# Kernel optimization log

Measured on AMD Instinct MI355X. Metric: run time of the kernel, lower is better.

## Reference

```python
import jax, jax.numpy as jnp
import numpy as np

jax.config.update("jax_enable_x64", True)

N_SPINS = 32
BATCH = 64
CPLX = jnp.complex128


def gen_v_from_zz_px(zz, PX=1):
    # zz: (n,) real +/-1 values -> isometry v: (2n, n) complex
    n = zz.shape[-1]
    N = 2 * n
    sgn = jnp.sign(zz)
    sgn = sgn.at[-1].set(-PX * sgn[-1])
    norm = 1.0 / jnp.sqrt(2.0)
    top = -1j * sgn * norm
    bot = (1.0 + 0j) * norm
    a_idx = 2 * jnp.arange(n) + 1
    b_idx = (2 * jnp.arange(n) + 2) % N
    col = jnp.arange(n)
    v = jnp.zeros((N, n), dtype=CPLX)
    v = v.at[a_idx, col].set(top)
    v = v.at[b_idx, col].set(bot)
    return v


def green_function_from_two(L, R):
    Lh = jnp.swapaxes(L.conj(), -1, -2)
    M = Lh @ R
    X = jnp.linalg.solve(M, Lh)
    gbar = R @ X
    N = gbar.shape[-1]
    I = jnp.eye(N, dtype=gbar.dtype)
    return I - 2 * gbar


def gen_green_init_s_proj(s, PX=1):
    zz_val = s * jnp.roll(s, -1, axis=-1)
    v = gen_v_from_zz_px(zz_val, PX)
    return v, green_function_from_two(v, v)


def green_function_from_s_state(s, state, PX=1):
    zz_val = s * jnp.roll(s, -1, axis=-1)
    v = gen_v_from_zz_px(zz_val, PX)
    return green_function_from_two(v, state)


def _householder_n(x, n):
    # x: (N,) complex column; n traced index. Returns reflector v, tau, alpha.
    arange = jnp.arange(x.size)
    xn = x[n]
    x = jnp.where(arange <= n, jnp.zeros_like(x), x)
    sigma = jnp.vdot(x, x)
    norm_x = jnp.sqrt(xn.conj() * xn + sigma)
    phase = jnp.where(xn == 0.0, 1.0, xn / jnp.abs(xn))
    vn = xn + phase * norm_x
    alpha = -phase * norm_x
    v = jnp.where(arange == n, vn, x)
    v = v / jnp.linalg.norm(v)
    cond = sigma == 0.0
    v = jnp.where(cond, jnp.zeros_like(x), v)
    tau = jnp.where(cond, 0, 2)
    alpha = jnp.where(cond, xn, alpha)
    return v, tau, alpha


def slog_pfaffian(A):
    # Sequential Householder tridiagonalization with running sign/log tracking.
    N = A.shape[0]

    def body(carry, i):
        A, sign_val, logpf = carry
        v, tau, alpha = _householder_n(A[:, i], i + 1)
        w = tau * (A @ v.conj())
        A = A + jnp.outer(v, w) - jnp.outer(w, v)
        logpf = logpf + jnp.log(jnp.abs(1 - tau)) + jnp.where(
            i % 2 == 0, jnp.log(jnp.abs(-alpha)), jnp.asarray(0.0, logpf.dtype))
        sign_val = sign_val * ((1 - tau) / jnp.abs(1 - tau)) * jnp.where(
            i % 2 == 0, -alpha / jnp.abs(-alpha), jnp.asarray(1.0, sign_val.dtype))
        return (A, sign_val, logpf), None

    init = (A, jnp.asarray(1.0, A.dtype), jnp.asarray(0.0, jnp.float64))
    (A, sign_val, logpf), _ = jax.lax.scan(body, init, jnp.arange(N - 2))
    logpf = logpf + jnp.log(jnp.abs(A[N - 2, N - 1]))
    sign_val = sign_val * (A[N - 2, N - 1] / jnp.abs(A[N - 2, N - 1]))
    return sign_val, logpf


def log_eta_propagation(G1, G2, logeta1, logeta2):
    logeta1 = jnp.asarray(logeta1)
    logeta2 = jnp.asarray(logeta2)
    A = (G1 - G1.T) * 0.5
    D = (G2 - G2.T) * 0.5
    ndim = G1.shape[0]
    I = jnp.eye(ndim, dtype=CPLX)
    pfmat = jnp.block([[A, -I], [I, D]])
    sign_pref = (-1) ** (ndim // 2)
    sign_pf, logabs_pf = slog_pfaffian(pfmat)
    combined_sign = jnp.asarray(sign_pref, dtype=CPLX) * sign_pf
    return logeta1 + logeta2 + jnp.log(combined_sign) + logabs_pf


def logeta_g_expH_from_H(H):
    H_herm = 1j * (H - H.T) / 2
    e, v = jnp.linalg.eigh(H_herm)
    green = jnp.real(v @ jnp.diag(1j * jnp.tan(e / 2.0)) @ v.conj().T)
    e_pos = e[: e.shape[-1] // 2]
    logeta = jnp.sum(jnp.log(jnp.cos(e_pos / 2.0).astype(CPLX)))
    expH = v @ jnp.diag(jnp.exp(-1j * e)) @ v.conj().T
    return logeta, green, expH


def majorana_minus_state(n, dtype=CPLX):
    N = 2 * n
    norm = jnp.array(1 / jnp.sqrt(2.0), dtype=dtype)
    k = jnp.arange(n)
    e_even = jax.nn.one_hot(2 * k, N, dtype=dtype).T
    e_odd = jax.nn.one_hot(2 * k + 1, N, dtype=dtype).T
    phase_even = jnp.where(k == n - 1, 1j, -1j).astype(dtype)
    return phase_even * norm * e_even + 1.0 * norm * e_odd


def majorana_plus_state(n, dtype=CPLX):
    N = 2 * n
    norm = jnp.array(1 / jnp.sqrt(2.0), dtype=dtype)
    k = jnp.arange(n)
    e_even = jax.nn.one_hot(2 * k, N, dtype=dtype).T
    e_odd = jax.nn.one_hot(2 * k + 1, N, dtype=dtype).T
    return -1j * norm * e_even + 1.0 * norm * e_odd


def setup_inputs() -> dict:
    key = jax.random.key(0)
    k1, k2, k3 = jax.random.split(key, 3)
    n, B = N_SPINS, BATCH
    # spin configurations +/- 1
    x = jnp.where(jax.random.uniform(k1, (B, n)) > 0.5, 1.0, -1.0).astype(jnp.float64)
    s0 = jnp.ones((n,), dtype=jnp.float64)
    H1 = 1e-4 * jax.random.normal(k2, (2 * n, 2 * n), dtype=jnp.float64)
    H2 = 1e-4 * jax.random.normal(k3, (2 * n, 2 * n), dtype=jnp.float64)
    return {"x": x, "s0": s0, "H1": H1, "H2": H2}


def reference(x, s0, H1, H2):
    n = x.shape[-1]
    plus_state = majorana_plus_state(n)
    minus_state = majorana_minus_state(n)
    v_plus, Gz_plus = gen_green_init_s_proj(s0, PX=1)
    v_minus, Gz_minus = gen_green_init_s_proj(s0, PX=-1)
    le_p, G_p, expH_p = logeta_g_expH_from_H(H1)
    le_m, G_m, expH_m = logeta_g_expH_from_H(H2)
    logeta_Ghz_plus = log_eta_propagation(G_p, Gz_plus, le_p, 0.0)
    Ghz_plus = green_function_from_two(v_plus, expH_p @ v_plus)
    logeta_Ghz_minus = log_eta_propagation(G_m, Gz_minus, le_m, 0.0)
    Ghz_minus = green_function_from_two(v_minus, expH_m @ v_minus)

    def batch_fun(_x):
        Gs_p = green_function_from_s_state(_x, plus_state, PX=1)
        Gs_m = green_function_from_s_state(_x, minus_state, PX=-1)
        lo_p = log_eta_propagation(Ghz_plus, Gs_p, logeta_Ghz_plus, 0.0)
        lo_m = log_eta_propagation(Ghz_minus, Gs_m, logeta_Ghz_minus, 0.0)
        stacked = jnp.stack(
            [lo_m, jnp.log(_x[-1].astype(CPLX) * s0[-1].astype(CPLX)) + lo_p], axis=0)
        return jax.scipy.special.logsumexp(stacked, axis=0)

    return jax.vmap(batch_fun)(x)
```

## Files before the change

kernel.cpp:

```cpp
#include <hip/hip_runtime.h>
#include <math.h>


typedef double2 dcx;
typedef float2 cf;
#define PI_ 3.14159265358979323846
#define SIDX16(i,j) (((i) << 6) | (((((j) >> 1) ^ ((i) & 31)) << 1) | ((j) & 1)))

__device__ __forceinline__ dcx dmk(double re, double im){ dcx c; c.x=re; c.y=im; return c; }
__device__ __forceinline__ dcx dmul(dcx a, dcx b){ return dmk(a.x*b.x - a.y*b.y, a.x*b.y + a.y*b.x); }

__device__ __forceinline__ double bf2d(unsigned short u){
  union { unsigned u; float f; } cv; cv.u = ((unsigned)u) << 16; return (double)cv.f;
}
__device__ __forceinline__ unsigned short d2bf(double v){
  float f = (float)v;
  union { float f; unsigned u; } cv; cv.f = f;
  unsigned u = cv.u;
  u = (u + 0x7FFFu + ((u >> 16) & 1u)) >> 16;
  return (unsigned short)u;
}
__device__ __forceinline__ int detect_mode(const void* p){
  unsigned w0 = *(const unsigned*)p;
  if ((w0 & 0x7FFFFFFFu) == 0x3F800000u) return 1;
  if ((w0 & 0x7FFFu) == 0x3F80u) return 0;
  return 2;
}
__device__ __forceinline__ double ldv(const void* p, int idx, int mode){
  if (mode == 0) return bf2d(((const unsigned short*)p)[idx]);
  if (mode == 1) return (double)((const float*)p)[idx];
  return ((const double*)p)[idx];
}
__device__ __forceinline__ double ldc(const double* p){
  return __hip_atomic_load(p, __ATOMIC_RELAXED, __HIP_MEMORY_SCOPE_AGENT);
}
__device__ __forceinline__ dcx ldc2(const dcx* p){
  dcx r; r.x = ldc(&p->x); r.y = ldc(&p->y); return r;
}

__device__ void mm64f_1024(float* C, const float* A, const float* B, float scale){
  const int t = threadIdx.x;
  const int w = t >> 6, L = t & 63;
  const int i = 4*w + (L >> 4);
  const int j4 = (L & 15) << 2;
  const float* Ar = A + i*64;
  float4 acc; acc.x = acc.y = acc.z = acc.w = 0.f;
  #pragma unroll 8
  for (int k = 0; k < 64; ++k) {
    float a = Ar[k];
    float4 b = *(const float4*)(B + k*64 + j4);
    acc.x += a*b.x; acc.y += a*b.y; acc.z += a*b.z; acc.w += a*b.w;
  }
  acc.x *= scale; acc.y *= scale; acc.z *= scale; acc.w *= scale;
  *(float4*)(C + i*64 + j4) = acc;
}

__global__ __launch_bounds__(1024) void pre_mat(
    const void* __restrict__ h1, const void* __restrict__ h2, const void* __restrict__ s0,
    cf* Apx, cf* Czpx, cf* AinvG, dcx* lec_base, int* cnt)
{
  const int px = blockIdx.x;
  const int t = threadIdx.x;
  const int lane = t & 63, wv = t >> 6;
  const float is2 = 0.70710678118654752440f;
  const int mode = detect_mode(s0);
  const void* H = (px == 0) ? h1 : h2;

  if (px == 0 && t == 0) *cnt = 0;

  __shared__ __align__(16) unsigned char SH[49664];
  float* Kf = (float*)SH;
  float* Ef = (float*)(SH + 16384);
  cf*   Rc  = (cf*)(SH + 32768);
  cf*   Msl = (cf*)(SH + 16384);
  cf*   Tsl = (cf*)(SH + 16384 + 8192);
  cf*   RMc = (cf*)SH;
  cf*   ALDS = (cf*)(SH + 16384);
  double* ssh = (double*)(SH + 49152);
  double* red = (double*)(SH + 49408);
  __shared__ double le_sh;

  if (t < 32) {
    double a = ldv(s0, t, mode);
    double b = ldv(s0, (t + 1) & 31, mode);
    double zz = a * b;
    double s = (zz >= 0.0) ? 1.0 : -1.0;
    if (t == 31) s = (px == 0) ? -s : s;
    ssh[t] = s;
  }
  double k2 = 0.0;
  for (int e = t; e < 4096; e += 1024) {
    int i = e >> 6, j = e & 63;
    float kv = (float)(0.5 * (ldv(H, i*64 + j, mode) - ldv(H, j*64 + i, mode)));
    Kf[e] = kv;
    k2 += (double)kv * (double)kv;
  }
  #pragma unroll
  for (int off = 32; off > 0; off >>= 1) k2 += __shfl_down(k2, off, 64);
  if (lane == 0) red[wv] = k2;
  __syncthreads();
  if (t == 0) {
    double acc = 0.0;
    #pragma unroll
    for (int w = 0; w < 16; ++w) acc += red[w];
    le_sh = -acc / 16.0;
  }
  mm64f_1024(Ef, Kf, Kf, 0.5f);
  __syncthreads();
  for (int e = t; e < 4096; e += 1024) {
    int i = e >> 6, j = e & 63;
    Ef[e] += Kf[e] + ((i == j) ? 1.f : 0.f);
  }
  __syncthreads();
  for (int e = t; e < 2048; e += 1024) {
    int r = e >> 5, k = e & 31;
    int a = 2*k + 1, b2 = (2*k + 2) & 63;
    cf z; z.x = Ef[r*64 + b2] * is2; z.y = -(float)ssh[k] * Ef[r*64 + a] * is2;
    Rc[e] = z;
  }
  __syncthreads();
  {
    int e = t;
    int c = e >> 5, k = e & 31;
    int a = 2*c + 1, b2 = (2*c + 2) & 63;
    cf Ra = Rc[a*32 + k], Rb = Rc[b2*32 + k];
    float s = (float)ssh[c];
    cf z; z.x = (-Ra.y*s + Rb.x)*is2; z.y = (Ra.x*s + Rb.y)*is2;
    Msl[e] = z;
  }
  __syncthreads();
  {
    int e = t;
    int i = e >> 5, j = e & 31;
    float ar = 0.f, ai = 0.f;
    for (int k = 0; k < 32; ++k) {
      cf d1 = Msl[i*32 + k]; if (k == i) d1.x -= 1.f;
      cf d2 = Msl[k*32 + j]; if (k == j) d2.x -= 1.f;
      ar += d1.x*d2.x - d1.y*d2.y;
      ai += d1.x*d2.y + d1.y*d2.x;
    }
    cf z; z.x = ar; z.y = ai;
    __syncthreads();
    cf m = Msl[e];
    cf w; w.x = ((i == j) ? 2.f : 0.f) - m.x + z.x; w.y = -m.y + z.y;
    Tsl[e] = w;
  }
  for (int e = t; e < 4096; e += 1024) {
    int r = e >> 6, c = e & 63;
    float vr = -0.5f * Kf[e];
    float vi = 0.f;
    if ((r & 1) && c == ((r + 1) & 63)) vi = (float)ssh[r >> 1];
    else if ((c & 1) && r == ((c + 1) & 63)) vi = -(float)ssh[c >> 1];
    cf z; z.x = vr; z.y = vi;
    Czpx[(size_t)px*4096 + e] = z;
  }
  __syncthreads();
  for (int e = t; e < 2048; e += 1024) {
    int r = e >> 5, j = e & 31;
    float ar = 0.f, ai = 0.f;
    for (int k = 0; k < 32; ++k) {
      cf a = Rc[r*32 + k], b = Tsl[k*32 + j];
      ar += a.x*b.x - a.y*b.y;
      ai += a.x*b.y + a.y*b.x;
    }
    cf z; z.x = ar; z.y = ai;
    RMc[e] = z;
  }
  __syncthreads();
  for (int e = t; e < 4096; e += 1024) {
    int r = e >> 6, j = e & 63;
    int cj, cr; cf uj, ur;
    if (j & 1) { cj = j >> 1; uj.x = 0.f; uj.y = (float)ssh[cj] * is2; }
    else { cj = ((j >> 1) + 31) & 31; uj.x = is2; uj.y = 0.f; }
    if (r & 1) { cr = r >> 1; ur.x = 0.f; ur.y = (float)ssh[cr] * is2; }
    else { cr = ((r >> 1) + 31) & 31; ur.x = is2; ur.y = 0.f; }
    cf m1 = RMc[r*32 + cj], m2 = RMc[j*32 + cr];
    cf t1; t1.x = m1.x*uj.x - m1.y*uj.y; t1.y = m1.x*uj.y + m1.y*uj.x;
    cf t2; t2.x = m2.x*ur.x - m2.y*ur.y; t2.y = m2.x*ur.y + m2.y*ur.x;
    cf z; z.x = t2.x - t1.x; z.y = t2.y - t1.y;
    Apx[(size_t)px*4096 + e] = z;
    ALDS[e] = z;
  }
  __syncthreads();
  for (int e = t; e < 4096; e += 1024) {
    int r = e >> 6, c = e & 63;
    int pr = (r & 1) ? ((r + 1) & 63) : ((r - 1) & 63);
    int pc = (c & 1) ? ((c + 1) & 63) : ((c - 1) & 63);
    float ar = (r & 1) ? (float)ssh[r >> 1] : -(float)ssh[((r - 1) & 63) >> 1];
    float ac = (c & 1) ? (float)ssh[c >> 1] : -(float)ssh[((c - 1) & 63) >> 1];
    cf Ap = ALDS[pr*64 + pc];
    cf d; d.x = Ap.x; d.y = Ap.y;
    if (c == pr) d.y += ar;
    float f = -ar * ac;
    cf z; z.x = f*d.x; z.y = f*d.y;
    if (c == pr) z.y += ar;
    AinvG[(size_t)px*4096 + e] = z;
  }
  if (t == 0) {
    double ps = 1.0;
    for (int k = 0; k < 32; ++k) ps *= ssh[k];
    double phDz = (ps > 0.0) ? PI_ : 0.0;
    lec_base[px] = dmk(le_sh, phDz);
  }
}

__device__ void pfPR64q(cf* S, float4* ubuf, double* lab_out, double* ph_out){
  const int t = threadIdx.x;
  const int l = t & 63;
  const int w = t >> 6;
  const int lmask = l & 31;
  const int rbase = l << 6;
  double prodr = 1.0, prodi = 0.0;
  int neg = 0, zflag = 0;
  for (int p = 0; p < 31; ++p) {
    const int l0 = 2*p;
    __syncthreads();
    cf b1 = S[SIDX16(l, l0)];
    cf b2 = S[SIDX16(l, l0+1)];
    cf a; a.x = __shfl(b2.x, l0, 64); a.y = __shfl(b2.y, l0, 64);
    float am2 = a.x*a.x + a.y*a.y;
    if (am2 < 1e-4f) {
      float val = (l >= l0+1) ? (b1.x*b1.x + b1.y*b1.y) : 0.f;
      unsigned pk = (__float_as_uint(val) & 0xFFFFFFC0u) | (unsigned)l;
      #pragma unroll
      for (int off = 32; off > 0; off >>= 1) {
        unsigned o = (unsigned)__shfl_xor((int)pk, off, 64);
        if (o > pk) pk = o;
      }
      int q = (int)(pk & 63u);
      if (q > l0+1) {
        __syncthreads();
        if (t < 64) {
          cf r1 = S[SIDX16(l0+1, t)], r2 = S[SIDX16(q, t)];
          S[SIDX16(l0+1, t)] = r2; S[SIDX16(q, t)] = r1;
        }
        __syncthreads();
        if (t < 64) {
          cf u1 = S[SIDX16(t, l0+1)], u2 = S[SIDX16(t, q)];
          S[SIDX16(t, l0+1)] = u2; S[SIDX16(t, q)] = u1;
        }
        __syncthreads();
        neg ^= 1;
      }
      b1 = S[SIDX16(l, l0)]; b2 = S[SIDX16(l, l0+1)];
      a.x = __shfl(b2.x, l0, 64); a.y = __shfl(b2.y, l0, 64);
      am2 = a.x*a.x + a.y*a.y;
    }
    {
      double nr = prodr*(double)a.x - prodi*(double)a.y;
      double ni = prodr*(double)a.y + prodi*(double)a.x;
      prodr = nr; prodi = ni;
    }
    if (am2 == 0.f) { zflag = 1; continue; }
    float rcp = 1.f/am2;
    cf iv; iv.x = a.x*rcp; iv.y = -a.y*rcp;
    cf w1, w2;
    w1.x = b1.x*iv.x - b1.y*iv.y; w1.y = b1.x*iv.y + b1.y*iv.x;
    w2.x = b2.x*iv.x - b2.y*iv.y; w2.y = b2.x*iv.y + b2.y*iv.x;
    float4 ub; ub.x = b1.x; ub.y = b1.y; ub.z = b2.x; ub.w = b2.y;
    ubuf[l] = ub;
    __syncthreads();
    const int lim = l0 + 2;
    const bool rowok = (l >= lim);
    #pragma unroll
    for (int jj = 0; jj < 8; ++jj) {
      int q2 = p + 1 + jj*4 + w;
      int qc = (q2 > 31) ? 31 : q2;
      float4 ua  = ubuf[2*qc];
      float4 ubx = ubuf[2*qc + 1];
      int idx = rbase | ((qc ^ lmask) << 1);
      float4 cur = *(float4*)(S + idx);
      cur.x += w2.x*ua.x  - w2.y*ua.y  - w1.x*ua.z  + w1.y*ua.w;
      cur.y += w2.x*ua.y  + w2.y*ua.x  - w1.x*ua.w  - w1.y*ua.z;
      cur.z += w2.x*ubx.x - w2.y*ubx.y - w1.x*ubx.z + w1.y*ubx.w;
      cur.w += w2.x*ubx.y + w2.y*ubx.x - w1.x*ubx.w - w1.y*ubx.z;
      if (rowok && q2 <= 31) *(float4*)(S + idx) = cur;
    }
  }
  __syncthreads();
  cf z = S[SIDX16(62, 63)];
  double nr = prodr*(double)z.x - prodi*(double)z.y;
  double ni = prodr*(double)z.y + prodi*(double)z.x;
  if (neg) { nr = -nr; ni = -ni; }
  double m2 = nr*nr + ni*ni;
  if (zflag || m2 == 0.0) { *lab_out = -23000.0; *ph_out = 0.0; }
  else { *lab_out = 0.5*log(m2); *ph_out = atan2(ni, nr); }
}

__device__ void final_body(const void* __restrict__ x, const void* __restrict__ s0,
                           const dcx* __restrict__ lec_base, const dcx* __restrict__ lecA,
                           const dcx* __restrict__ lo, void* __restrict__ out, int out_size)
{
  int b = threadIdx.x;
  if (b >= 64) return;
  const int mode = detect_mode(x);
  double L[2], P[2];
  #pragma unroll
  for (int px = 0; px < 2; ++px) {
    dcx base = lec_base[px];
    dcx eA = ldc2(&lecA[px]);
    dcx eC = ldc2(&lecA[2 + px]);
    dcx l  = ldc2(&lo[px*64 + b]);
    L[px] = base.x + eA.x + eC.x + l.x;
    P[px] = base.y + eA.y + eC.y + l.y;
  }
  dcx t1 = dmk(L[1], P[1]);
  dcx t2 = dmk(L[0], P[0]);
  double v = ldv(x, b*32 + 31, mode) * ldv(s0, 31, mode);
  t2.x += log(fabs(v));
  if (v < 0.0) t2.y += PI_;
  double mr = fmax(t1.x, t2.x);
  double e1 = exp(t1.x - mr), e2 = exp(t2.x - mr);
  double zr = e1 * cos(t1.y) + e2 * cos(t2.y);
  double zi = e1 * sin(t1.y) + e2 * sin(t2.y);
  double outr = mr + 0.5 * log(zr*zr + zi*zi);
  double outi = atan2(zi, zr);
  if (mode == 0) {
    unsigned short* o = (unsigned short*)out;
    if (out_size >= 128) { o[2*b] = d2bf(outr); o[2*b + 1] = d2bf(outi); }
    else o[b] = d2bf(outr);
  } else {
    float* o = (float*)out;
    if (out_size >= 128) { o[2*b] = (float)outr; o[2*b + 1] = (float)outi; }
    else o[b] = (float)outr;
  }
}

__global__ __launch_bounds__(256, 1) void batch_kernel(
    const void* __restrict__ x, const void* __restrict__ s0,
    const cf* __restrict__ Apx, const cf* __restrict__ Czpx,
    const cf* __restrict__ AinvG, const dcx* __restrict__ lec_base,
    dcx* lo, dcx* lecA, int* cnt, void* out, int out_size)
{
  __shared__ __align__(16) unsigned char SH[36608];
  cf* Sp      = (cf*)SH;
  double* ssh = (double*)(SH + 32768);
  dcx* rho    = (dcx*)(SH + 33024);
  dcx* uu     = (dcx*)(SH + 34048);
  int* cidx   = (int*)(SH + 35072);
  float* pref = (float*)(SH + 35328);
  float4* ubuf = (float4*)(SH + 35472);
  __shared__ int is_last;
  const int t = threadIdx.x;
  const int pb = blockIdx.x;
  const double inv_sqrt2 = 0.70710678118654752440;

  if (pb >= 128) {
    const int idx = pb - 128;
    const cf* src = (idx < 2) ? (Apx + (size_t)idx*4096) : (Czpx + (size_t)(idx-2)*4096);
    for (int e = t; e < 4096; e += 256) {
      int i = e >> 6, j = e & 63;
      Sp[SIDX16(i, j)] = src[((i + 1) & 63)*64 + ((j + 1) & 63)];
    }
  } else {
    const int px = pb >> 6, b = pb & 63;
    const int mode = detect_mode(x);

    if (t < 32) {
      double a = ldv(x, b*32 + t, mode);
      double b2 = ldv(x, b*32 + ((t + 1) & 31), mode);
      double zz = a * b2;
      double s = (zz >= 0.0) ? 1.0 : -1.0;
      if (t == 31) s = (px == 0) ? -s : s;
      ssh[t] = s;
    }
    __syncthreads();
    if (t < 64) {
      int r = t;
      if (r & 1) rho[r] = dmk(inv_sqrt2, 0.0);
      else {
        int k = r >> 1;
        double pim = -inv_sqrt2;
        if (px == 1 && k == 31) pim = inv_sqrt2;
        rho[r] = dmk(0.0, pim);
      }
      int j = t;
      if (j & 1) { cidx[j] = j >> 1; uu[j] = dmk(0.0, ssh[j >> 1] * inv_sqrt2); }
      else { cidx[j] = ((j >> 1) + 31) & 31; uu[j] = dmk(inv_sqrt2, 0.0); }
    }
    if (t == 0) {
      float pp = 1.f;
      pref[0] = 1.f;
      for (int c = 0; c < 32; ++c) {
        float q = (px == 1 && c == 30) ? 1.f : -1.f;
        pp *= q * (float)ssh[c];
        pref[c + 1] = pp;
      }
    }
    __syncthreads();
    for (int e = t; e < 4096; e += 256) {
      int a = e >> 6, bb = e & 63;
      int r1 = bb >> 1, c1 = cidx[a];
      float f1 = ((c1 < r1) ? -1.f : 1.f) * (((c1 - r1) & 1) ? -1.f : 1.f)
                 * pref[r1] * pref[c1] * (float)ssh[c1];
      int r2 = a >> 1, c2 = cidx[bb];
      float f2 = ((c2 < r2) ? -1.f : 1.f) * (((c2 - r2) & 1) ? -1.f : 1.f)
                 * pref[r2] * pref[c2] * (float)ssh[c2];
      dcx m1 = dmk(0.0, -(double)f1);
      dcx m2 = dmk(0.0, -(double)f2);
      dcx t1 = dmul(dmul(rho[bb], uu[a]), m1);
      dcx t2 = dmul(dmul(rho[a], uu[bb]), m2);
      cf av = AinvG[(size_t)px*4096 + e];
      cf z;
      z.x = (float)((double)av.x + t1.x - t2.x);
      z.y = (float)((double)av.y + t1.y - t2.y);
      Sp[SIDX16(a, bb)] = z;
    }
  }
  double lab, ph;
  pfPR64q(Sp, ubuf, &lab, &ph);
  if (t == 0) {
    if (pb >= 128) lecA[pb - 128] = dmk(lab, ph + PI_);
    else lo[pb] = dmk(lab, ph);
    __threadfence();
    int old = atomicAdd(cnt, 1);
    is_last = (old == 131) ? 1 : 0;
  }
  __syncthreads();
  if (is_last) {
    __threadfence();
    final_body(x, s0, lec_base, lecA, lo, out, out_size);
  }
}

extern "C" void kernel_launch(void* const* d_in, const int* in_sizes, int n_in,
                              void* d_out, int out_size, void* d_ws, size_t ws_size,
                              hipStream_t stream)
{
  const void* x  = d_in[0];
  const void* s0 = d_in[1];
  const void* h1 = d_in[2];
  const void* h2 = d_in[3];

  cf*  Apx   = (cf*)d_ws;
  cf*  Czpx  = Apx + 8192;
  cf*  AinvG = Czpx + 8192;
  dcx* lec_base = (dcx*)(AinvG + 8192);
  dcx* lecA  = lec_base + 2;
  dcx* lo    = lecA + 4;
  int* cnt   = (int*)(lo + 128);

  pre_mat<<<dim3(2), dim3(1024), 0, stream>>>(h1, h2, s0, Apx, Czpx, AinvG, lec_base, cnt);
  batch_kernel<<<dim3(132), dim3(256), 0, stream>>>(x, s0, Apx, Czpx, AinvG, lec_base,
                                                    lo, lecA, cnt, d_out, out_size);
}
```

Measured before the change: 117.7 us.

## Fuse two Pfaffian elimination steps per barrier round with pivot-free fast path

Adds a new Pfaffian routine that processes two 2x2 elimination steps per outer iteration without pivoting. It double-buffers the next pivot rows and columns in shared memory, which halves the number of block-wide barriers and the passes over the matrix. If a pivot is too small, the matrix is rebuilt and the original pivoting routine runs as a fallback. This costs extra shared memory and code size, and the fallback path repeats the build work.

```diff
diff --git a/kernel.cpp b/kernel.cpp
--- a/kernel.cpp
+++ b/kernel.cpp
@@ -204,7 +204,7 @@
   }
 }
 
-__device__ void pfPR64q(cf* S, float4* ubuf, double* lab_out, double* ph_out){
+__device__ __noinline__ void pfPR64q(cf* S, float4* ubuf, double* lab_out, double* ph_out){
   const int t = threadIdx.x;
   const int l = t & 63;
   const int w = t >> 6;
@@ -287,6 +287,208 @@
   else { *lab_out = 0.5*log(m2); *ph_out = atan2(ni, nr); }
 }
 
+__device__ int pfPR64b(cf* S, float4* bufB0, float4* bufB1, float4* bufC0, float4* bufC1,
+                       float4* ubufX, double* lab_out, double* ph_out){
+  const int t = threadIdx.x;
+  const int l = t & 63;
+  const int wid = t >> 6;
+  const int lmask = l & 31;
+  const int rbase = l << 6;
+  double prodr = 1.0, prodi = 0.0;
+  int bad = 0;
+  __syncthreads();
+  if (t < 64) {
+    bufB0[l] = *(float4*)(S + (rbase | ((0 ^ lmask) << 1)));
+    bufC0[l] = *(float4*)(S + (rbase | ((1 ^ lmask) << 1)));
+  }
+  cf w1, w2, w1p, w2p;
+  float4 Cp;
+  for (int P = 0; P < 15; ++P) {
+    float4* bB = (P & 1) ? bufB1 : bufB0;
+    float4* bC = (P & 1) ? bufC1 : bufC0;
+    float4* nB = (P & 1) ? bufB0 : bufB1;
+    float4* nC = (P & 1) ? bufC0 : bufC1;
+    __syncthreads();
+    if (!bad) {
+      float4 bb = bB[l];
+      float4 cc = bC[l];
+      float4 aA = bB[4*P];
+      cf a1; a1.x = aA.z; a1.y = aA.w;
+      float am1 = a1.x*a1.x + a1.y*a1.y;
+      if (am1 < 1e-4f) { bad = 1; }
+      else {
+        double nr = prodr*(double)a1.x - prodi*(double)a1.y;
+        double ni = prodr*(double)a1.y + prodi*(double)a1.x;
+        prodr = nr; prodi = ni;
+        float rcp = 1.f/am1;
+        cf iv; iv.x = a1.x*rcp; iv.y = -a1.y*rcp;
+        float m = (l >= 4*P + 2) ? 1.f : 0.f;
+        w1.x = (bb.x*iv.x - bb.y*iv.y)*m; w1.y = (bb.x*iv.y + bb.y*iv.x)*m;
+        w2.x = (bb.z*iv.x - bb.w*iv.y)*m; w2.y = (bb.z*iv.y + bb.w*iv.x)*m;
+        float4 uC2 = bB[4*P + 2];
+        float4 uC3 = bB[4*P + 3];
+        Cp.x = cc.x + w2.x*uC2.x - w2.y*uC2.y - w1.x*uC2.z + w1.y*uC2.w;
+        Cp.y = cc.y + w2.x*uC2.y + w2.y*uC2.x - w1.x*uC2.w - w1.y*uC2.z;
+        Cp.z = cc.z + w2.x*uC3.x - w2.y*uC3.y - w1.x*uC3.z + w1.y*uC3.w;
+        Cp.w = cc.w + w2.x*uC3.y + w2.y*uC3.x - w1.x*uC3.w - w1.y*uC3.z;
+        if (wid == 0) ubufX[l] = Cp;
+      }
+    }
+    __syncthreads();
+    if (!bad) {
+      float4 aB = ubufX[4*P + 2];
+      cf a2; a2.x = aB.z; a2.y = aB.w;
+      float am2 = a2.x*a2.x + a2.y*a2.y;
+      if (am2 < 1e-4f) { bad = 1; }
+      else {
+        double nr = prodr*(double)a2.x - prodi*(double)a2.y;
+        double ni = prodr*(double)a2.y + prodi*(double)a2.x;
+        prodr = nr; prodi = ni;
+        float rcp = 1.f/am2;
+        cf iv; iv.x = a2.x*rcp; iv.y = -a2.y*rcp;
+        float m2 = (l >= 4*P + 4) ? 1.f : 0.f;
+        w1p.x = (Cp.x*iv.x - Cp.y*iv.y)*m2; w1p.y = (Cp.x*iv.y + Cp.y*iv.x)*m2;
+        w2p.x = (Cp.z*iv.x - Cp.w*iv.y)*m2; w2p.y = (Cp.z*iv.y + Cp.w*iv.x)*m2;
+        const bool rowok = (l >= 4*P + 2);
+        #pragma unroll
+        for (int jj = 0; jj < 8; ++jj) {
+          int q2 = 2*P + 2 + jj*4 + wid;
+          int qc = (q2 > 31) ? 31 : q2;
+          float4 uA0 = bB[2*qc];
+          float4 uA1 = bB[2*qc + 1];
+          float4 uX0 = ubufX[2*qc];
+          float4 uX1 = ubufX[2*qc + 1];
+          int idx = rbase | ((qc ^ lmask) << 1);
+          float4 cur = *(float4*)(S + idx);
+          cur.x += w2.x*uA0.x - w2.y*uA0.y - w1.x*uA0.z + w1.y*uA0.w
+                 + w2p.x*uX0.x - w2p.y*uX0.y - w1p.x*uX0.z + w1p.y*uX0.w;
+          cur.y += w2.x*uA0.y + w2.y*uA0.x - w1.x*uA0.w - w1.y*uA0.z
+                 + w2p.x*uX0.y + w2p.y*uX0.x - w1p.x*uX0.w - w1p.y*uX0.z;
+          cur.z += w2.x*uA1.x - w2.y*uA1.y - w1.x*uA1.z + w1.y*uA1.w
+                 + w2p.x*uX1.x - w2p.y*uX1.y - w1p.x*uX1.z + w1p.y*uX1.w;
+          cur.w += w2.x*uA1.y + w2.y*uA1.x - w1.x*uA1.w - w1.y*uA1.z
+                 + w2p.x*uX1.y + w2p.y*uX1.x - w1p.x*uX1.w - w1p.y*uX1.z;
+          if (rowok && q2 <= 31) {
+            *(float4*)(S + idx) = cur;
+            if (jj == 0) {
+              if (wid == 0) nB[l] = cur;
+              else if (wid == 1) nC[l] = cur;
+            }
+          }
+        }
+      }
+    }
+  }
+  __syncthreads();
+  if (!bad) {
+    float4 bb = bufB1[l];
+    float4 aA = bufB1[60];
+    cf a; a.x = aA.z; a.y = aA.w;
+    float am = a.x*a.x + a.y*a.y;
+    if (am < 1e-4f) { bad = 1; }
+    else {
+      double nr = prodr*(double)a.x - prodi*(double)a.y;
+      double ni = prodr*(double)a.y + prodi*(double)a.x;
+      prodr = nr; prodi = ni;
+      float rcp = 1.f/am;
+      cf iv; iv.x = a.x*rcp; iv.y = -a.y*rcp;
+      float m = (l >= 62) ? 1.f : 0.f;
+      cf v1, v2;
+      v1.x = (bb.x*iv.x - bb.y*iv.y)*m; v1.y = (bb.x*iv.y + bb.y*iv.x)*m;
+      v2.x = (bb.z*iv.x - bb.w*iv.y)*m; v2.y = (bb.z*iv.y + bb.w*iv.x)*m;
+      if (wid == 0) {
+        float4 u0 = bufB1[62];
+        float4 u1 = bufB1[63];
+        int idx = rbase | ((31 ^ lmask) << 1);
+        float4 cur = *(float4*)(S + idx);
+        cur.x += v2.x*u0.x - v2.y*u0.y - v1.x*u0.z + v1.y*u0.w;
+        cur.y += v2.x*u0.y + v2.y*u0.x - v1.x*u0.w - v1.y*u0.z;
+        cur.z += v2.x*u1.x - v2.y*u1.y - v1.x*u1.z + v1.y*u1.w;
+        cur.w += v2.x*u1.y + v2.y*u1.x - v1.x*u1.w - v1.y*u1.z;
+        if (l >= 62) *(float4*)(S + idx) = cur;
+      }
+    }
+  }
+  __syncthreads();
+  if (bad) return 1;
+  cf z = S[SIDX16(62, 63)];
+  double nr = prodr*(double)z.x - prodi*(double)z.y;
+  double ni = prodr*(double)z.y + prodi*(double)z.x;
+  double m2 = nr*nr + ni*ni;
+  if (m2 == 0.0) { *lab_out = -23000.0; *ph_out = 0.0; }
+  else { *lab_out = 0.5*log(m2); *ph_out = atan2(ni, nr); }
+  return 0;
+}
+
+__device__ __noinline__ void build_S(cf* Sp, int pb, const void* x,
+    const cf* Apx, const cf* Czpx, const cf* AinvG,
+    double* ssh, dcx* rho, dcx* uu, int* cidx, float* pref)
+{
+  const int t = threadIdx.x;
+  const double inv_sqrt2 = 0.70710678118654752440;
+  if (pb >= 128) {
+    const int idx = pb - 128;
+    const cf* src = (idx < 2) ? (Apx + (size_t)idx*4096) : (Czpx + (size_t)(idx-2)*4096);
+    for (int e = t; e < 4096; e += 256) {
+      int i = e >> 6, j = e & 63;
+      Sp[SIDX16(i, j)] = src[((i + 1) & 63)*64 + ((j + 1) & 63)];
+    }
+    return;
+  }
+  const int px = pb >> 6, b = pb & 63;
+  const int mode = detect_mode(x);
+  if (t < 32) {
+    double a = ldv(x, b*32 + t, mode);
+    double b2 = ldv(x, b*32 + ((t + 1) & 31), mode);
+    double zz = a * b2;
+    double s = (zz >= 0.0) ? 1.0 : -1.0;
+    if (t == 31) s = (px == 0) ? -s : s;
+    ssh[t] = s;
+  }
+  __syncthreads();
+  if (t < 64) {
+    int r = t;
+    if (r & 1) rho[r] = dmk(inv_sqrt2, 0.0);
+    else {
+      int k = r >> 1;
+      double pim = -inv_sqrt2;
+      if (px == 1 && k == 31) pim = inv_sqrt2;
+      rho[r] = dmk(0.0, pim);
+    }
+    int j = t;
+    if (j & 1) { cidx[j] = j >> 1; uu[j] = dmk(0.0, ssh[j >> 1] * inv_sqrt2); }
+    else { cidx[j] = ((j >> 1) + 31) & 31; uu[j] = dmk(inv_sqrt2, 0.0); }
+  }
+  if (t == 0) {
+    float pp = 1.f;
+    pref[0] = 1.f;
+    for (int c = 0; c < 32; ++c) {
+      float q = (px == 1 && c == 30) ? 1.f : -1.f;
+      pp *= q * (float)ssh[c];
+      pref[c + 1] = pp;
+    }
+  }
+  __syncthreads();
+  for (int e = t; e < 4096; e += 256) {
+    int a = e >> 6, bb = e & 63;
+    int r1 = bb >> 1, c1 = cidx[a];
+    float f1 = ((c1 < r1) ? -1.f : 1.f) * (((c1 - r1) & 1) ? -1.f : 1.f)
+               * pref[r1] * pref[c1] * (float)ssh[c1];
+    int r2 = a >> 1, c2 = cidx[bb];
+    float f2 = ((c2 < r2) ? -1.f : 1.f) * (((c2 - r2) & 1) ? -1.f : 1.f)
+               * pref[r2] * pref[c2] * (float)ssh[c2];
+    dcx m1 = dmk(0.0, -(double)f1);
+    dcx m2 = dmk(0.0, -(double)f2);
+    dcx t1 = dmul(dmul(rho[bb], uu[a]), m1);
+    dcx t2 = dmul(dmul(rho[a], uu[bb]), m2);
+    cf av = AinvG[(size_t)px*4096 + e];
+    cf z;
+    z.x = (float)((double)av.x + t1.x - t2.x);
+    z.y = (float)((double)av.y + t1.y - t2.y);
+    Sp[SIDX16(a, bb)] = z;
+  }
+}
+
 __device__ void final_body(const void* __restrict__ x, const void* __restrict__ s0,
                            const dcx* __restrict__ lec_base, const dcx* __restrict__ lecA,
                            const dcx* __restrict__ lo, void* __restrict__ out, int out_size)
@@ -332,83 +534,31 @@
     const cf* __restrict__ AinvG, const dcx* __restrict__ lec_base,
     dcx* lo, dcx* lecA, int* cnt, void* out, int out_size)
 {
-  __shared__ __align__(16) unsigned char SH[36608];
+  __shared__ __align__(16) unsigned char SH[40704];
   cf* Sp      = (cf*)SH;
   double* ssh = (double*)(SH + 32768);
   dcx* rho    = (dcx*)(SH + 33024);
   dcx* uu     = (dcx*)(SH + 34048);
   int* cidx   = (int*)(SH + 35072);
   float* pref = (float*)(SH + 35328);
-  float4* ubuf = (float4*)(SH + 35472);
+  float4* bufB0 = (float4*)(SH + 35472);
+  float4* bufB1 = (float4*)(SH + 36496);
+  float4* bufC0 = (float4*)(SH + 37520);
+  float4* bufC1 = (float4*)(SH + 38544);
+  float4* ubufX = (float4*)(SH + 39568);
   __shared__ int is_last;
   const int t = threadIdx.x;
   const int pb = blockIdx.x;
-  const double inv_sqrt2 = 0.70710678118654752440;
-
-  if (pb >= 128) {
-    const int idx = pb - 128;
-    const cf* src = (idx < 2) ? (Apx + (size_t)idx*4096) : (Czpx + (size_t)(idx-2)*4096);
-    for (int e = t; e < 4096; e += 256) {
-      int i = e >> 6, j = e & 63;
-      Sp[SIDX16(i, j)] = src[((i + 1) & 63)*64 + ((j + 1) & 63)];
-    }
-  } else {
-    const int px = pb >> 6, b = pb & 63;
-    const int mode = detect_mode(x);
-
-    if (t < 32) {
-      double a = ldv(x, b*32 + t, mode);
-      double b2 = ldv(x, b*32 + ((t + 1) & 31), mode);
-      double zz = a * b2;
-      double s = (zz >= 0.0) ? 1.0 : -1.0;
-      if (t == 31) s = (px == 0) ? -s : s;
-      ssh[t] = s;
-    }
+
+  build_S(Sp, pb, x, Apx, Czpx, AinvG, ssh, rho, uu, cidx, pref);
+
+  double lab, ph;
+  int bad = pfPR64b(Sp, bufB0, bufB1, bufC0, bufC1, ubufX, &lab, &ph);
+  if (bad) {
     __syncthreads();
-    if (t < 64) {
-      int r = t;
-      if (r & 1) rho[r] = dmk(inv_sqrt2, 0.0);
-      else {
-        int k = r >> 1;
-        double pim = -inv_sqrt2;
-        if (px == 1 && k == 31) pim = inv_sqrt2;
-        rho[r] = dmk(0.0, pim);
-      }
-      int j = t;
-      if (j & 1) { cidx[j] = j >> 1; uu[j] = dmk(0.0, ssh[j >> 1] * inv_sqrt2); }
-      else { cidx[j] = ((j >> 1) + 31) & 31; uu[j] = dmk(inv_sqrt2, 0.0); }
-    }
-    if (t == 0) {
-      float pp = 1.f;
-      pref[0] = 1.f;
-      for (int c = 0; c < 32; ++c) {
-        float q = (px == 1 && c == 30) ? 1.f : -1.f;
-        pp *= q * (float)ssh[c];
-        pref[c + 1] = pp;
-      }
-    }
-    __syncthreads();
-    for (int e = t; e < 4096; e += 256) {
-      int a = e >> 6, bb = e & 63;
-      int r1 = bb >> 1, c1 = cidx[a];
-      float f1 = ((c1 < r1) ? -1.f : 1.f) * (((c1 - r1) & 1) ? -1.f : 1.f)
-                 * pref[r1] * pref[c1] * (float)ssh[c1];
-      int r2 = a >> 1, c2 = cidx[bb];
-      float f2 = ((c2 < r2) ? -1.f : 1.f) * (((c2 - r2) & 1) ? -1.f : 1.f)
-                 * pref[r2] * pref[c2] * (float)ssh[c2];
-      dcx m1 = dmk(0.0, -(double)f1);
-      dcx m2 = dmk(0.0, -(double)f2);
-      dcx t1 = dmul(dmul(rho[bb], uu[a]), m1);
-      dcx t2 = dmul(dmul(rho[a], uu[bb]), m2);
-      cf av = AinvG[(size_t)px*4096 + e];
-      cf z;
-      z.x = (float)((double)av.x + t1.x - t2.x);
-      z.y = (float)((double)av.y + t1.y - t2.y);
-      Sp[SIDX16(a, bb)] = z;
-    }
-  }
-  double lab, ph;
-  pfPR64q(Sp, ubuf, &lab, &ph);
+    build_S(Sp, pb, x, Apx, Czpx, AinvG, ssh, rho, uu, cidx, pref);
+    pfPR64q(Sp, ubufX, &lab, &ph);
+  }
   if (t == 0) {
     if (pb >= 128) lecA[pb - 128] = dmk(lab, ph + PI_);
     else lo[pb] = dmk(lab, ph);
```

Measured after the change: 129.5 us. 10.0% more time.

## Add optimistic no-pivot Pfaffian path with double-buffered pivot rows, pivoting fallback

Applied to the files above, without the earlier changes.

Adds a fast Pfaffian elimination that assumes no pivoting is needed. The next pivot row goes into a double-buffered shared ubuf, which removes the per-step shuffle and argmax reductions of the pivoted version. If a small pivot shows up, the block rebuilds the matrix and reruns the original pivoting routine. Matrix construction is split out into a noinline helper. This trades a possible double cost on bad inputs and a slightly larger shared-memory footprint for cheaper iterations in the common case.

```diff
diff --git a/kernel.cpp b/kernel.cpp
--- a/kernel.cpp
+++ b/kernel.cpp
@@ -204,7 +204,7 @@
   }
 }
 
-__device__ void pfPR64q(cf* S, float4* ubuf, double* lab_out, double* ph_out){
+__device__ __noinline__ void pfPR64q(cf* S, float4* ubuf, double* lab_out, double* ph_out){
   const int t = threadIdx.x;
   const int l = t & 63;
   const int w = t >> 6;
@@ -287,6 +287,138 @@
   else { *lab_out = 0.5*log(m2); *ph_out = atan2(ni, nr); }
 }
 
+__device__ int pfPR64pl(cf* S, float4* ubuf , double* lab_out, double* ph_out){
+  const int t = threadIdx.x;
+  const int l = t & 63;
+  const int w = t >> 6;
+  const int lmask = l & 31;
+  const int rbase = l << 6;
+  double prodr = 1.0, prodi = 0.0;
+  int bad = 0;
+  __syncthreads();
+  if (t < 64) {
+    ubuf[l] = *(float4*)(S + (rbase | ((0 ^ lmask) << 1)));
+  }
+  for (int p = 0; p < 31; ++p) {
+    float4* bP = ubuf + ((p & 1) << 6);
+    float4* bN = ubuf + (((p + 1) & 1) << 6);
+    __syncthreads();
+    if (bad) continue;
+    float4 bb = bP[l];
+    float4 aA = bP[2*p];
+    cf a; a.x = aA.z; a.y = aA.w;
+    float am2 = a.x*a.x + a.y*a.y;
+    if (am2 < 1e-4f) { bad = 1; continue; }
+    {
+      double nr = prodr*(double)a.x - prodi*(double)a.y;
+      double ni = prodr*(double)a.y + prodi*(double)a.x;
+      prodr = nr; prodi = ni;
+    }
+    float rcp = 1.f/am2;
+    cf iv; iv.x = a.x*rcp; iv.y = -a.y*rcp;
+    const bool rowok = (l >= 2*p + 2);
+    float m = rowok ? 1.f : 0.f;
+    cf w1, w2;
+    w1.x = (bb.x*iv.x - bb.y*iv.y)*m; w1.y = (bb.x*iv.y + bb.y*iv.x)*m;
+    w2.x = (bb.z*iv.x - bb.w*iv.y)*m; w2.y = (bb.z*iv.y + bb.w*iv.x)*m;
+    #pragma unroll
+    for (int jj = 0; jj < 8; ++jj) {
+      int q2 = p + 1 + jj*4 + w;
+      int qc = (q2 > 31) ? 31 : q2;
+      float4 ua  = bP[2*qc];
+      float4 ubx = bP[2*qc + 1];
+      int idx = rbase | ((qc ^ lmask) << 1);
+      float4 cur = *(float4*)(S + idx);
+      cur.x += w2.x*ua.x  - w2.y*ua.y  - w1.x*ua.z  + w1.y*ua.w;
+      cur.y += w2.x*ua.y  + w2.y*ua.x  - w1.x*ua.w  - w1.y*ua.z;
+      cur.z += w2.x*ubx.x - w2.y*ubx.y - w1.x*ubx.z + w1.y*ubx.w;
+      cur.w += w2.x*ubx.y + w2.y*ubx.x - w1.x*ubx.w - w1.y*ubx.z;
+      if (rowok && q2 <= 31) {
+        *(float4*)(S + idx) = cur;
+        if (jj == 0 && w == 0) bN[l] = cur;
+      }
+    }
+  }
+  __syncthreads();
+  if (bad) return 1;
+  cf z = S[SIDX16(62, 63)];
+  double nr = prodr*(double)z.x - prodi*(double)z.y;
+  double ni = prodr*(double)z.y + prodi*(double)z.x;
+  double m2 = nr*nr + ni*ni;
+  if (m2 == 0.0) { *lab_out = -23000.0; *ph_out = 0.0; }
+  else { *lab_out = 0.5*log(m2); *ph_out = atan2(ni, nr); }
+  return 0;
+}
+
+__device__ __noinline__ void build_S(cf* Sp, int pb, const void* x,
+    const cf* Apx, const cf* Czpx, const cf* AinvG,
+    double* ssh, dcx* rho, dcx* uu, int* cidx, float* pref)
+{
+  const int t = threadIdx.x;
+  const double inv_sqrt2 = 0.70710678118654752440;
+  if (pb >= 128) {
+    const int idx = pb - 128;
+    const cf* src = (idx < 2) ? (Apx + (size_t)idx*4096) : (Czpx + (size_t)(idx-2)*4096);
+    for (int e = t; e < 4096; e += 256) {
+      int i = e >> 6, j = e & 63;
+      Sp[SIDX16(i, j)] = src[((i + 1) & 63)*64 + ((j + 1) & 63)];
+    }
+    return;
+  }
+  const int px = pb >> 6, b = pb & 63;
+  const int mode = detect_mode(x);
+  if (t < 32) {
+    double a = ldv(x, b*32 + t, mode);
+    double b2 = ldv(x, b*32 + ((t + 1) & 31), mode);
+    double zz = a * b2;
+    double s = (zz >= 0.0) ? 1.0 : -1.0;
+    if (t == 31) s = (px == 0) ? -s : s;
+    ssh[t] = s;
+  }
+  __syncthreads();
+  if (t < 64) {
+    int r = t;
+    if (r & 1) rho[r] = dmk(inv_sqrt2, 0.0);
+    else {
+      int k = r >> 1;
+      double pim = -inv_sqrt2;
+      if (px == 1 && k == 31) pim = inv_sqrt2;
+      rho[r] = dmk(0.0, pim);
+    }
+    int j = t;
+    if (j & 1) { cidx[j] = j >> 1; uu[j] = dmk(0.0, ssh[j >> 1] * inv_sqrt2); }
+    else { cidx[j] = ((j >> 1) + 31) & 31; uu[j] = dmk(inv_sqrt2, 0.0); }
+  }
+  if (t == 0) {
+    float pp = 1.f;
+    pref[0] = 1.f;
+    for (int c = 0; c < 32; ++c) {
+      float q = (px == 1 && c == 30) ? 1.f : -1.f;
+      pp *= q * (float)ssh[c];
+      pref[c + 1] = pp;
+    }
+  }
+  __syncthreads();
+  for (int e = t; e < 4096; e += 256) {
+    int a = e >> 6, bb = e & 63;
+    int r1 = bb >> 1, c1 = cidx[a];
+    float f1 = ((c1 < r1) ? -1.f : 1.f) * (((c1 - r1) & 1) ? -1.f : 1.f)
+               * pref[r1] * pref[c1] * (float)ssh[c1];
+    int r2 = a >> 1, c2 = cidx[bb];
+    float f2 = ((c2 < r2) ? -1.f : 1.f) * (((c2 - r2) & 1) ? -1.f : 1.f)
+               * pref[r2] * pref[c2] * (float)ssh[c2];
+    dcx m1 = dmk(0.0, -(double)f1);
+    dcx m2 = dmk(0.0, -(double)f2);
+    dcx t1 = dmul(dmul(rho[bb], uu[a]), m1);
+    dcx t2 = dmul(dmul(rho[a], uu[bb]), m2);
+    cf av = AinvG[(size_t)px*4096 + e];
+    cf z;
+    z.x = (float)((double)av.x + t1.x - t2.x);
+    z.y = (float)((double)av.y + t1.y - t2.y);
+    Sp[SIDX16(a, bb)] = z;
+  }
+}
+
 __device__ void final_body(const void* __restrict__ x, const void* __restrict__ s0,
                            const dcx* __restrict__ lec_base, const dcx* __restrict__ lecA,
                            const dcx* __restrict__ lo, void* __restrict__ out, int out_size)
@@ -332,7 +464,7 @@
     const cf* __restrict__ AinvG, const dcx* __restrict__ lec_base,
     dcx* lo, dcx* lecA, int* cnt, void* out, int out_size)
 {
-  __shared__ __align__(16) unsigned char SH[36608];
+  __shared__ __align__(16) unsigned char SH[37520];
   cf* Sp      = (cf*)SH;
   double* ssh = (double*)(SH + 32768);
   dcx* rho    = (dcx*)(SH + 33024);
@@ -343,72 +475,16 @@
   __shared__ int is_last;
   const int t = threadIdx.x;
   const int pb = blockIdx.x;
-  const double inv_sqrt2 = 0.70710678118654752440;
-
-  if (pb >= 128) {
-    const int idx = pb - 128;
-    const cf* src = (idx < 2) ? (Apx + (size_t)idx*4096) : (Czpx + (size_t)(idx-2)*4096);
-    for (int e = t; e < 4096; e += 256) {
-      int i = e >> 6, j = e & 63;
-      Sp[SIDX16(i, j)] = src[((i + 1) & 63)*64 + ((j + 1) & 63)];
-    }
-  } else {
-    const int px = pb >> 6, b = pb & 63;
-    const int mode = detect_mode(x);
-
-    if (t < 32) {
-      double a = ldv(x, b*32 + t, mode);
-      double b2 = ldv(x, b*32 + ((t + 1) & 31), mode);
-      double zz = a * b2;
-      double s = (zz >= 0.0) ? 1.0 : -1.0;
-      if (t == 31) s = (px == 0) ? -s : s;
-      ssh[t] = s;
-    }
+
+  build_S(Sp, pb, x, Apx, Czpx, AinvG, ssh, rho, uu, cidx, pref);
+
+  double lab, ph;
+  int bad = pfPR64pl(Sp, ubuf, &lab, &ph);
+  if (bad) {
     __syncthreads();
-    if (t < 64) {
-      int r = t;
-      if (r & 1) rho[r] = dmk(inv_sqrt2, 0.0);
-      else {
-        int k = r >> 1;
-        double pim = -inv_sqrt2;
-        if (px == 1 && k == 31) pim = inv_sqrt2;
-        rho[r] = dmk(0.0, pim);
-      }
-      int j = t;
-      if (j & 1) { cidx[j] = j >> 1; uu[j] = dmk(0.0, ssh[j >> 1] * inv_sqrt2); }
-      else { cidx[j] = ((j >> 1) + 31) & 31; uu[j] = dmk(inv_sqrt2, 0.0); }
-    }
-    if (t == 0) {
-      float pp = 1.f;
-      pref[0] = 1.f;
-      for (int c = 0; c < 32; ++c) {
-        float q = (px == 1 && c == 30) ? 1.f : -1.f;
-        pp *= q * (float)ssh[c];
-        pref[c + 1] = pp;
-      }
-    }
-    __syncthreads();
-    for (int e = t; e < 4096; e += 256) {
-      int a = e >> 6, bb = e & 63;
-      int r1 = bb >> 1, c1 = cidx[a];
-      float f1 = ((c1 < r1) ? -1.f : 1.f) * (((c1 - r1) & 1) ? -1.f : 1.f)
-                 * pref[r1] * pref[c1] * (float)ssh[c1];
-      int r2 = a >> 1, c2 = cidx[bb];
-      float f2 = ((c2 < r2) ? -1.f : 1.f) * (((c2 - r2) & 1) ? -1.f : 1.f)
-                 * pref[r2] * pref[c2] * (float)ssh[c2];
-      dcx m1 = dmk(0.0, -(double)f1);
-      dcx m2 = dmk(0.0, -(double)f2);
-      dcx t1 = dmul(dmul(rho[bb], uu[a]), m1);
-      dcx t2 = dmul(dmul(rho[a], uu[bb]), m2);
-      cf av = AinvG[(size_t)px*4096 + e];
-      cf z;
-      z.x = (float)((double)av.x + t1.x - t2.x);
-      z.y = (float)((double)av.y + t1.y - t2.y);
-      Sp[SIDX16(a, bb)] = z;
-    }
-  }
-  double lab, ph;
-  pfPR64q(Sp, ubuf, &lab, &ph);
+    build_S(Sp, pb, x, Apx, Czpx, AinvG, ssh, rho, uu, cidx, pref);
+    pfPR64q(Sp, ubuf, &lab, &ph);
+  }
   if (t == 0) {
     if (pb >= 128) lecA[pb - 128] = dmk(lab, ph + PI_);
     else lo[pb] = dmk(lab, ph);
```

Result: slower. 132.4 us (+12.4%).
